# Performance work log

Hardware: AMD Instinct MI355X
Metric: run time of the kernel (lower is better)

The kernel has to match this reference:

```python
import jax, jax.numpy as jnp
import numpy as np

B, N, E, IN = 16, 4096, 65536, 128
FILTERS = [256, 256, 128]


def setup_inputs() -> dict:
    key = jax.random.key(0)
    ks = jax.random.split(key, 12)
    inp = {
        "x": jax.random.normal(ks[0], (B, N, IN), dtype=jnp.float32),
        "edge_index": jax.random.randint(ks[1], (B, 2, E), 0, N, dtype=jnp.int32),
        "edge_weight": jax.random.uniform(ks[2], (B, E), dtype=jnp.float32),
        "mask": jax.random.randint(ks[3], (B, N), 0, 2, dtype=jnp.int32),
    }
    dims = [IN] + FILTERS
    for i in range(3):
        inp[f"W{i+1}"] = jax.random.normal(ks[4 + 2 * i], (dims[i], dims[i + 1]), dtype=jnp.float32) / np.sqrt(dims[i]).astype(np.float32)
        inp[f"b{i+1}"] = 0.01 * jax.random.normal(ks[5 + 2 * i], (dims[i + 1],), dtype=jnp.float32)
    return inp


def _gcn_layer(x, ei, ew, valid, W, b):
    # GCNConv(add_self_loops=False, normalize=False):
    #   h = x @ W; out[v] = sum_{(u,v)} ew * h[u]; out += b (valid rows only)
    h = x @ W  # [N, d_out]
    u, v = ei[0], ei[1]
    evalid = valid[u] & valid[v]            # drop edges touching masked-out nodes
    w = jnp.where(evalid, ew, 0.0)
    agg = jnp.zeros_like(h).at[v].add(w[:, None] * h[u])
    return jnp.where(valid[:, None], agg + b, 0.0)


def reference(x, edge_index, edge_weight, mask, W1, b1, W2, b2, W3, b3):
    valid = mask > 0  # [B, N] bool
    out = x
    for W, b in ((W1, b1), (W2, b2), (W3, b3)):
        out = jax.vmap(_gcn_layer, in_axes=(0, 0, 0, 0, None, None))(
            out, edge_index, edge_weight, valid, W, b)
        out = jax.nn.relu(out)  # dropout p=0.0 -> identity
    return out
```

## Files before the change

kernel.cpp:

```cpp
#include <hip/hip_runtime.h>

static constexpr int BATCH = 16;
static constexpr int NNODE = 4096;
static constexpr int NEDGE = 65536;
static constexpr int ROWS  = BATCH * NNODE;
static constexpr int CAP   = 2432;
static constexpr int PM    = BATCH * CAP;

typedef _Float16 half8  __attribute__((ext_vector_type(8)));
typedef _Float16 half4v __attribute__((ext_vector_type(4)));
typedef _Float16 half2v __attribute__((ext_vector_type(2)));
typedef float    f32x4  __attribute__((ext_vector_type(4)));
typedef float    f32x2  __attribute__((ext_vector_type(2)));

#define GP(p) (const __attribute__((address_space(1))) void*)(p)
#define LP(p) (__attribute__((address_space(3))) void*)(p)


__global__ __launch_bounds__(256) void count_kernel(
    const int* __restrict__ ei, const int* __restrict__ mask,
    int* __restrict__ counts)
{
    const int idx = blockIdx.x * 256 + threadIdx.x;
    const int b = idx >> 16;
    const int e = idx & (NEDGE - 1);
    const int* eib = ei + (size_t)b * 2 * NEDGE;
    const int u = eib[e];
    const int v = eib[NEDGE + e];
    const int mrow = b * NNODE;
    if (mask[mrow + u] != 0 && mask[mrow + v] != 0)
        atomicAdd(&counts[mrow + v], 1);
}

__global__ __launch_bounds__(256) void scan_compact_kernel(
    const int* __restrict__ counts, const int* __restrict__ mask,
    int* __restrict__ row_start, int* __restrict__ cursor,
    int* __restrict__ vlist, int* __restrict__ cidx, int* __restrict__ validN)
{
    __shared__ int sums[256];
    const int t = threadIdx.x;

    if (blockIdx.x < BATCH) {
        const int b = blockIdx.x;
        const int* c = counts + b * NNODE;
        int* rs = row_start + b * (NNODE + 1);
        int* cu = cursor + b * NNODE;

        int local[16]; int s = 0;
        #pragma unroll
        for (int i = 0; i < 16; ++i) { local[i] = c[t * 16 + i]; s += local[i]; }
        sums[t] = s;
        __syncthreads();
        for (int off = 1; off < 256; off <<= 1) {
            int v = (t >= off) ? sums[t - off] : 0;
            __syncthreads();
            sums[t] += v;
            __syncthreads();
        }
        int run = (t == 0) ? 0 : sums[t - 1];
        #pragma unroll
        for (int i = 0; i < 16; ++i) { rs[t * 16 + i] = run; cu[t * 16 + i] = run; run += local[i]; }
        if (t == 255) rs[NNODE] = run;
    } else {
        const int b = blockIdx.x - BATCH;
        const int* mb = mask + b * NNODE;
        for (int i = t; i < CAP; i += 256) vlist[b * CAP + i] = 0;

        int loc[16]; int s = 0;
        #pragma unroll
        for (int i = 0; i < 16; ++i) { loc[i] = (mb[t * 16 + i] != 0); s += loc[i]; }
        sums[t] = s;
        __syncthreads();
        for (int off = 1; off < 256; off <<= 1) {
            int v = (t >= off) ? sums[t - off] : 0;
            __syncthreads();
            sums[t] += v;
            __syncthreads();
        }
        int run = (t == 0) ? 0 : sums[t - 1];
        #pragma unroll
        for (int i = 0; i < 16; ++i) {
            const int n = t * 16 + i;
            if (loc[i]) {
                if (run < CAP) { vlist[b * CAP + run] = n; cidx[b * NNODE + n] = b * CAP + run; }
                ++run;
            } else {
                cidx[b * NNODE + n] = 0;
            }
        }
        if (t == 255) validN[b] = run;
    }
}

__global__ __launch_bounds__(256) void fill_prep_kernel(
    const int* __restrict__ ei, const float* __restrict__ ew,
    const int* __restrict__ mask, const int* __restrict__ cidx,
    int* __restrict__ cursor, unsigned int* __restrict__ bkt,
    const float* __restrict__ X, const int* __restrict__ vlist,
    const float* __restrict__ W1, const float* __restrict__ W2,
    const float* __restrict__ W3,
    _Float16* __restrict__ X16c, _Float16* __restrict__ Wt1,
    _Float16* __restrict__ Wt2, _Float16* __restrict__ Wt3)
{
    const int blk = blockIdx.x;
    if (blk < 4096) {
        const int idx = blk * 256 + threadIdx.x;
        const int b = idx >> 16;
        const int e = idx & (NEDGE - 1);
        const int* eib = ei + (size_t)b * 2 * NEDGE;
        const int u = eib[e];
        const int v = eib[NEDGE + e];
        const int mrow = b * NNODE;
        if (mask[mrow + u] != 0 && mask[mrow + v] != 0) {
            const _Float16 w = (_Float16)ew[(size_t)b * NEDGE + e];
            const unsigned short wb = __builtin_bit_cast(unsigned short, w);
            const unsigned uc = (unsigned)cidx[mrow + u];
            const int pos = atomicAdd(&cursor[mrow + v], 1);
            bkt[(size_t)b * NEDGE + pos] = ((unsigned)wb << 16) | uc;
        }
    } else {
        const int idx = (blk - 4096) * 256 + threadIdx.x;
        if (idx < PM * 32) {
            const int row = idx >> 5;
            const int c4  = idx & 31;
            const int b   = row / CAP;
            const int v   = vlist[row];
            const float4 s = *(const float4*)&X[((size_t)b * NNODE + v) * 128 + c4 * 4];
            half4v h = {(_Float16)s.x, (_Float16)s.y, (_Float16)s.z, (_Float16)s.w};
            *(half4v*)&X16c[(size_t)row * 128 + c4 * 4] = h;
        } else {
            const int i = idx - PM * 32;
            if (i < 32768) {
                int k = i >> 8, n = i & 255;
                Wt1[n * 128 + k] = (_Float16)W1[i];
            } else if (i < 98304) {
                int j = i - 32768;
                int k = j >> 8, n = j & 255;
                Wt2[n * 256 + k] = (_Float16)W2[j];
            } else {
                int j = i - 98304;
                int k = j >> 7, n = j & 127;
                Wt3[n * 256 + k] = (_Float16)W3[j];
            }
        }
    }
}

template<int K, int N, bool EPI>
__global__ __launch_bounds__(256, 3) void gemm_full(
    const _Float16* __restrict__ Xc,
    const _Float16* __restrict__ Wt,
    const float* __restrict__ bias,
    _Float16* __restrict__ Hc)
{
    constexpr int NCH  = CAP / 64;
    constexpr int NPAN = K / 32;
    constexpr int NW   = N / 4;
    constexpr int NI   = NW / 16;
    constexpr int RST  = NW + 8;
    __shared__ _Float16 A16[NPAN * 64 * 32];

    const int tid  = threadIdx.x;
    const int lane = tid & 63;
    const int wave = tid >> 6;
    const int quad = lane >> 4;
    const int l15  = lane & 15;

    const int xcd  = blockIdx.x & 7;
    const int j    = blockIdx.x >> 3;
    const int batch = 2 * xcd + (j >= NCH);
    const int tile  = (j >= NCH) ? j - NCH : j;
    const size_t bm = (size_t)batch * CAP + (size_t)tile * 64;

    const int srow = tid >> 2;
    const int sch  = (tid & 3) * 8;
    #pragma unroll
    for (int pp = 0; pp < NPAN; ++pp)
        __builtin_amdgcn_global_load_lds(
            GP(Xc + (bm + srow) * K + pp * 32 + sch),
            LP(A16 + pp * 2048 + tid * 8), 16, 0, 0);
    __syncthreads();

    f32x4 acc[4][NI];
    #pragma unroll
    for (int mi = 0; mi < 4; ++mi)
        #pragma unroll
        for (int ni = 0; ni < NI; ++ni) acc[mi][ni] = (f32x4)0.0f;

    const _Float16* ap = A16 + l15 * 32 + quad * 8;
    const _Float16* wp = Wt + (size_t)(wave * NW + l15) * K + quad * 8;

    #pragma unroll
    for (int pp = 0; pp < NPAN; ++pp) {
        half8 af[4], bf[NI];
        #pragma unroll
        for (int mi = 0; mi < 4; ++mi)
            af[mi] = *(const half8*)(ap + pp * 2048 + mi * 16 * 32);
        #pragma unroll
        for (int ni = 0; ni < NI; ++ni)
            bf[ni] = *(const half8*)(wp + (size_t)ni * 16 * K + pp * 32);
        #pragma unroll
        for (int mi = 0; mi < 4; ++mi)
            #pragma unroll
            for (int ni = 0; ni < NI; ++ni)
                acc[mi][ni] = __builtin_amdgcn_mfma_f32_16x16x32_f16(
                    bf[ni], af[mi], acc[mi][ni], 0, 0, 0);
    }
    __syncthreads();

    _Float16* stg = A16 + wave * 16 * RST;
    const int rr = lane >> 2;
    const int c0 = lane & 3;
    #pragma unroll
    for (int mi = 0; mi < 4; ++mi) {
        #pragma unroll
        for (int ni = 0; ni < NI; ++ni) {
            f32x4 v = acc[mi][ni];
            half4v o;
            if (EPI) {
                const f32x4 bv = *(const f32x4*)&bias[wave * NW + ni * 16 + quad * 4];
                #pragma unroll
                for (int r = 0; r < 4; ++r) o[r] = (_Float16)fmaxf(v[r] + bv[r], 0.0f);
            } else {
                #pragma unroll
                for (int r = 0; r < 4; ++r) o[r] = (_Float16)v[r];
            }
            *(half4v*)&stg[l15 * RST + ni * 16 + quad * 4] = o;
        }
        const size_t grow = bm + mi * 16 + rr;
        _Float16* hp = &Hc[grow * N + wave * NW];
        #pragma unroll
        for (int c = 0; c < NI / 2; ++c) {
            const int ch = (c0 + 4 * c) * 8;
            half8 v = *(const half8*)&stg[rr * RST + ch];
            *(half8*)(hp + ch) = v;
        }
    }
}

__global__ __launch_bounds__(256, 3) void gemm23_kernel(
    const _Float16* __restrict__ Xc,
    const _Float16* __restrict__ Wt2,
    const _Float16* __restrict__ Wt3,
    const float* __restrict__ b2,
    _Float16* __restrict__ H3)
{
    constexpr int K    = 256;
    constexpr int NPAN = K / 32;
    constexpr int NCH  = CAP / 64;
    __shared__ _Float16 A16[NPAN * 64 * 32];

    const int tid  = threadIdx.x;
    const int lane = tid & 63;
    const int wave = tid >> 6;
    const int quad = lane >> 4;
    const int l15  = lane & 15;

    const int xcd  = blockIdx.x & 7;
    const int j    = blockIdx.x >> 3;
    const int batch = 2 * xcd + (j >= NCH);
    const int tile  = (j >= NCH) ? j - NCH : j;
    const size_t bm = (size_t)batch * CAP + (size_t)tile * 64;

    const int srow = tid >> 2;
    const int sch  = (tid & 3) * 8;
    #pragma unroll
    for (int pp = 0; pp < NPAN; ++pp)
        __builtin_amdgcn_global_load_lds(
            GP(Xc + (bm + srow) * K + pp * 32 + sch),
            LP(A16 + pp * 2048 + tid * 8), 16, 0, 0);
    __syncthreads();

    f32x4 acc[4][4];
    #pragma unroll
    for (int mi = 0; mi < 4; ++mi)
        #pragma unroll
        for (int ni = 0; ni < 4; ++ni) acc[mi][ni] = (f32x4)0.0f;

    const _Float16* ap = A16 + l15 * 32 + quad * 8;
    const _Float16* wp = Wt2 + (size_t)(wave * 64 + l15) * K + quad * 8;

    #pragma unroll
    for (int pp = 0; pp < NPAN; ++pp) {
        half8 af[4], bf[4];
        #pragma unroll
        for (int mi = 0; mi < 4; ++mi)
            af[mi] = *(const half8*)(ap + pp * 2048 + mi * 16 * 32);
        #pragma unroll
        for (int ni = 0; ni < 4; ++ni)
            bf[ni] = *(const half8*)(wp + (size_t)ni * 16 * K + pp * 32);
        #pragma unroll
        for (int mi = 0; mi < 4; ++mi)
            #pragma unroll
            for (int ni = 0; ni < 4; ++ni)
                acc[mi][ni] = __builtin_amdgcn_mfma_f32_16x16x32_f16(
                    bf[ni], af[mi], acc[mi][ni], 0, 0, 0);
    }
    __syncthreads();

    #pragma unroll
    for (int mi = 0; mi < 4; ++mi) {
        const int row = mi * 16 + l15;
        #pragma unroll
        for (int ni = 0; ni < 4; ++ni) {
            const int col = wave * 64 + ni * 16 + quad * 4;
            const f32x4 bv = *(const f32x4*)&b2[col];
            f32x4 v = acc[mi][ni];
            half4v o;
            #pragma unroll
            for (int r = 0; r < 4; ++r) o[r] = (_Float16)fmaxf(v[r] + bv[r], 0.0f);
            *(half4v*)&A16[(col >> 5) * 2048 + row * 32 + (col & 31)] = o;
        }
    }
    __syncthreads();

    f32x4 acc2[4][2];
    #pragma unroll
    for (int mi = 0; mi < 4; ++mi)
        #pragma unroll
        for (int ni = 0; ni < 2; ++ni) acc2[mi][ni] = (f32x4)0.0f;

    const _Float16* wp3 = Wt3 + (size_t)(wave * 32 + l15) * K + quad * 8;
    #pragma unroll
    for (int pp = 0; pp < NPAN; ++pp) {
        half8 af[4], bf[2];
        #pragma unroll
        for (int mi = 0; mi < 4; ++mi)
            af[mi] = *(const half8*)(ap + pp * 2048 + mi * 16 * 32);
        #pragma unroll
        for (int ni = 0; ni < 2; ++ni)
            bf[ni] = *(const half8*)(wp3 + (size_t)ni * 16 * K + pp * 32);
        #pragma unroll
        for (int mi = 0; mi < 4; ++mi)
            #pragma unroll
            for (int ni = 0; ni < 2; ++ni)
                acc2[mi][ni] = __builtin_amdgcn_mfma_f32_16x16x32_f16(
                    bf[ni], af[mi], acc2[mi][ni], 0, 0, 0);
    }
    __syncthreads();

    constexpr int RST = 40;
    _Float16* stg = A16 + wave * 16 * RST;
    const int rr = lane >> 2;
    const int c0 = lane & 3;
    #pragma unroll
    for (int mi = 0; mi < 4; ++mi) {
        #pragma unroll
        for (int ni = 0; ni < 2; ++ni) {
            f32x4 v = acc2[mi][ni];
            half4v o;
            #pragma unroll
            for (int r = 0; r < 4; ++r) o[r] = (_Float16)v[r];
            *(half4v*)&stg[l15 * RST + ni * 16 + quad * 4] = o;
        }
        const size_t grow = bm + mi * 16 + rr;
        _Float16* hp = &H3[grow * 128 + wave * 32];
        {
            const int ch = c0 * 8;
            half8 v = *(const half8*)&stg[rr * RST + ch];
            *(half8*)(hp + ch) = v;
        }
    }
}


__global__ __launch_bounds__(256) void gather_x(
    const int* __restrict__ row_start, const unsigned int* __restrict__ bkt,
    const _Float16* __restrict__ X,
    const int* __restrict__ vlist, const int* __restrict__ validN,
    _Float16* __restrict__ OUT)
{
    constexpr int NU = CAP / 4;
    const int tid  = threadIdx.x;
    const int lane = tid & 63;
    const int wave = tid >> 6;

    const int xcd  = blockIdx.x & 7;
    const int jj   = blockIdx.x >> 3;
    const int batch = 2 * xcd + (jj >= NU);
    const int unit  = (jj >= NU) ? jj - NU : jj;

    const int j = unit * 4 + wave;
    if (j >= validN[batch]) return;
    const int g = batch * CAP + j;
    const int v = vlist[g];

    const int* rs = row_start + batch * (NNODE + 1);
    const int s = rs[v], e = rs[v + 1];
    const unsigned* bk = bkt + (size_t)batch * NEDGE;
    const _Float16* Hb = X + lane * 2;

    float acc[2] = {};
    for (int i = s; i < e; i += 8) {
        const int cnt = e - i;
        unsigned pk[8];
        #pragma unroll
        for (int t = 0; t < 8; ++t) pk[t] = bk[i + t];
        const unsigned u0 = pk[0] & 0xffffu;
        float wj[8]; const _Float16* hp[8];
        #pragma unroll
        for (int t = 0; t < 8; ++t) {
            const bool ok = (t < cnt);
            const unsigned u = ok ? (pk[t] & 0xffffu) : u0;
            wj[t] = ok ? (float)__builtin_bit_cast(_Float16, (unsigned short)(pk[t] >> 16)) : 0.0f;
            hp[t] = Hb + (size_t)u * 128;
        }
        half2v hv[8];
        #pragma unroll
        for (int t = 0; t < 8; ++t) hv[t] = *(const half2v*)hp[t];
        #pragma unroll
        for (int t = 0; t < 8; ++t)
            #pragma unroll
            for (int c = 0; c < 2; ++c) acc[c] += wj[t] * (float)hv[t][c];
    }
    half2v o = {(_Float16)acc[0], (_Float16)acc[1]};
    *(half2v*)&OUT[(size_t)g * 128 + lane * 2] = o;
}

__global__ __launch_bounds__(256) void gather_agg(
    const int* __restrict__ row_start, const unsigned int* __restrict__ bkt,
    const _Float16* __restrict__ H,
    const int* __restrict__ vlist, const int* __restrict__ validN,
    _Float16* __restrict__ OUT)
{
    constexpr int NU = CAP / 4;
    const int tid  = threadIdx.x;
    const int lane = tid & 63;
    const int wave = tid >> 6;

    const int xcd  = blockIdx.x & 7;
    const int jj   = blockIdx.x >> 3;
    const int batch = 2 * xcd + (jj >= NU);
    const int unit  = (jj >= NU) ? jj - NU : jj;

    const int j = unit * 4 + wave;
    if (j >= validN[batch]) return;
    const int g = batch * CAP + j;
    const int v = vlist[g];

    const int* rs = row_start + batch * (NNODE + 1);
    const int s = rs[v], e = rs[v + 1];
    const unsigned* bk = bkt + (size_t)batch * NEDGE;
    const _Float16* Hb = H + lane * 4;

    float acc[4] = {};
    for (int i = s; i < e; i += 8) {
        const int cnt = e - i;
        unsigned pk[8];
        #pragma unroll
        for (int t = 0; t < 8; ++t) pk[t] = bk[i + t];
        const unsigned u0 = pk[0] & 0xffffu;
        float wj[8]; const _Float16* hp[8];
        #pragma unroll
        for (int t = 0; t < 8; ++t) {
            const bool ok = (t < cnt);
            const unsigned u = ok ? (pk[t] & 0xffffu) : u0;
            wj[t] = ok ? (float)__builtin_bit_cast(_Float16, (unsigned short)(pk[t] >> 16)) : 0.0f;
            hp[t] = Hb + (size_t)u * 256;
        }
        half4v hv[8];
        #pragma unroll
        for (int t = 0; t < 8; ++t) hv[t] = *(const half4v*)hp[t];
        #pragma unroll
        for (int t = 0; t < 8; ++t)
            #pragma unroll
            for (int c = 0; c < 4; ++c) acc[c] += wj[t] * (float)hv[t][c];
    }
    half4v o;
    #pragma unroll
    for (int c = 0; c < 4; ++c) o[c] = (_Float16)acc[c];
    *(half4v*)&OUT[(size_t)g * 256 + lane * 4] = o;
}

__global__ __launch_bounds__(256) void gather_final(
    const int* __restrict__ row_start, const unsigned int* __restrict__ bkt,
    const _Float16* __restrict__ H,
    const int* __restrict__ mask, const float* __restrict__ bias,
    float* __restrict__ OUT)
{
    constexpr int NU = NNODE / 4;
    const int tid  = threadIdx.x;
    const int lane = tid & 63;
    const int wave = tid >> 6;

    const int xcd  = blockIdx.x & 7;
    const int jj   = blockIdx.x >> 3;
    const int batch = 2 * xcd + (jj >= NU);
    const int unit  = (jj >= NU) ? jj - NU : jj;

    const int n = unit * 4 + wave;
    const int mrow = batch * NNODE + n;

    float acc[2] = {};
    if (mask[mrow] != 0) {
        const int* rs = row_start + batch * (NNODE + 1);
        const int s = rs[n], e = rs[n + 1];
        const unsigned* bk = bkt + (size_t)batch * NEDGE;
        const _Float16* Hb = H + lane * 2;

        for (int i = s; i < e; i += 8) {
            const int cnt = e - i;
            unsigned pk[8];
            #pragma unroll
            for (int t = 0; t < 8; ++t) pk[t] = bk[i + t];
            const unsigned u0 = pk[0] & 0xffffu;
            float wj[8]; const _Float16* hp[8];
            #pragma unroll
            for (int t = 0; t < 8; ++t) {
                const bool ok = (t < cnt);
                const unsigned u = ok ? (pk[t] & 0xffffu) : u0;
                wj[t] = ok ? (float)__builtin_bit_cast(_Float16, (unsigned short)(pk[t] >> 16)) : 0.0f;
                hp[t] = Hb + (size_t)u * 128;
            }
            half2v hv[8];
            #pragma unroll
            for (int t = 0; t < 8; ++t) hv[t] = *(const half2v*)hp[t];
            #pragma unroll
            for (int t = 0; t < 8; ++t)
                #pragma unroll
                for (int c = 0; c < 2; ++c) acc[c] += wj[t] * (float)hv[t][c];
        }
        #pragma unroll
        for (int c = 0; c < 2; ++c)
            acc[c] = fmaxf(acc[c] + bias[lane * 2 + c], 0.0f);
    }
    f32x2 o = {acc[0], acc[1]};
    *(f32x2*)&OUT[(size_t)mrow * 128 + lane * 2] = o;
}

extern "C" void kernel_launch(void* const* d_in, const int* in_sizes, int n_in,
                              void* d_out, int out_size, void* d_ws, size_t ws_size,
                              hipStream_t stream) {
    const float* x    = (const float*)d_in[0];
    const int*   ei   = (const int*)  d_in[1];
    const float* ew   = (const float*)d_in[2];
    const int*   mask = (const int*)  d_in[3];
    const float* W1   = (const float*)d_in[4];
    const float* b1   = (const float*)d_in[5];
    const float* W2   = (const float*)d_in[6];
    const float* b2   = (const float*)d_in[7];
    const float* W3   = (const float*)d_in[8];
    const float* b3   = (const float*)d_in[9];
    float* out = (float*)d_out;

    char* ws = (char*)d_ws;
    _Float16* X16c = (_Float16*)(ws);
    _Float16* AggX = (_Float16*)(ws + (10u << 20));
    _Float16* H3c  = AggX;
    _Float16* Ac   = (_Float16*)(ws + (20u << 20));
    _Float16* AggA = (_Float16*)(ws + (40u << 20));
    unsigned int* bkt = (unsigned int*)(ws + (60u << 20));
    _Float16* Wt1  = (_Float16*)(ws + (64u << 20));
    _Float16* Wt2  = Wt1 + 128 * 256;
    _Float16* Wt3  = Wt2 + 256 * 256;
    int* counts    = (int*)(Wt3 + 256 * 128);
    int* row_start = counts + ROWS;
    int* cursor    = row_start + BATCH * (NNODE + 1);
    int* cidx      = cursor + ROWS;
    int* vlist     = cidx + ROWS;
    int* validN    = vlist + PM;

    const dim3 blk(256);
    const int edgeBlocks = BATCH * NEDGE / 256;

    hipMemsetAsync(counts, 0, (size_t)ROWS * sizeof(int), stream);
    count_kernel<<<edgeBlocks, blk, 0, stream>>>(ei, mask, counts);
    scan_compact_kernel<<<2 * BATCH, blk, 0, stream>>>(counts, mask, row_start, cursor,
                                                       vlist, cidx, validN);
    const int prepBlocks = (PM * 32 + 131072) / 256;
    fill_prep_kernel<<<edgeBlocks + prepBlocks, blk, 0, stream>>>(
        ei, ew, mask, cidx, cursor, bkt, x, vlist, W1, W2, W3,
        X16c, Wt1, Wt2, Wt3);

    const int gemmBlocks = PM / 64;
    const int midBlocks  = PM / 4;
    const int finBlocks  = ROWS / 4;

    gather_x<<<midBlocks, blk, 0, stream>>>(row_start, bkt, X16c, vlist, validN, AggX);
    gemm_full<128, 256, true><<<gemmBlocks, blk, 0, stream>>>(AggX, Wt1, b1, Ac);

    gather_agg<<<midBlocks, blk, 0, stream>>>(row_start, bkt, Ac, vlist, validN, AggA);
    gemm23_kernel<<<gemmBlocks, blk, 0, stream>>>(AggA, Wt2, Wt3, b2, H3c);

    gather_final<<<finBlocks, blk, 0, stream>>>(row_start, bkt, H3c, mask, b3, out);
}
```

Measured before the change: 228.0 us.

## Fuse neighbor gathers into GEMM kernels and use fixed-capacity per-node edge buckets

Replaces the count, prefix-scan and CSR fill passes with one build kernel that scatters each valid edge into a fixed 64-slot bucket per destination node. The per-node cursor doubles as the degree. The separate gather kernels for layers 1 and 2 are folded into the GEMM kernels: each block aggregates its 64 compacted rows straight into shared memory before running the matrix multiply, and writes results scattered to full node-indexed buffers. This removes several launches and the round trips through intermediate aggregated buffers. In exchange, fewer waves do the gather serially, and edges beyond 64 per node are silently dropped.

Result: faster. 221.5 us (-2.9%).

```diff
diff --git a/kernel.cpp b/kernel.cpp
--- a/kernel.cpp
+++ b/kernel.cpp
@@ -6,6 +6,7 @@
 static constexpr int ROWS  = BATCH * NNODE;
 static constexpr int CAP   = 2432;
 static constexpr int PM    = BATCH * CAP;
+static constexpr int DCAP  = 64;
 
 typedef _Float16 half8  __attribute__((ext_vector_type(8)));
 typedef _Float16 half4v __attribute__((ext_vector_type(4)));
@@ -13,98 +14,22 @@
 typedef float    f32x4  __attribute__((ext_vector_type(4)));
 typedef float    f32x2  __attribute__((ext_vector_type(2)));
 
-#define GP(p) (const __attribute__((address_space(1))) void*)(p)
-#define LP(p) (__attribute__((address_space(3))) void*)(p)
-
-
-__global__ __launch_bounds__(256) void count_kernel(
-    const int* __restrict__ ei, const int* __restrict__ mask,
-    int* __restrict__ counts)
-{
-    const int idx = blockIdx.x * 256 + threadIdx.x;
-    const int b = idx >> 16;
-    const int e = idx & (NEDGE - 1);
-    const int* eib = ei + (size_t)b * 2 * NEDGE;
-    const int u = eib[e];
-    const int v = eib[NEDGE + e];
-    const int mrow = b * NNODE;
-    if (mask[mrow + u] != 0 && mask[mrow + v] != 0)
-        atomicAdd(&counts[mrow + v], 1);
-}
-
-__global__ __launch_bounds__(256) void scan_compact_kernel(
-    const int* __restrict__ counts, const int* __restrict__ mask,
-    int* __restrict__ row_start, int* __restrict__ cursor,
-    int* __restrict__ vlist, int* __restrict__ cidx, int* __restrict__ validN)
+__global__ __launch_bounds__(256) void build_kernel(
+    const int* __restrict__ ei, const float* __restrict__ ew,
+    const int* __restrict__ mask, const float* __restrict__ X,
+    const float* __restrict__ W1, const float* __restrict__ W2,
+    const float* __restrict__ W3,
+    int* __restrict__ cursor, unsigned int* __restrict__ bkt,
+    _Float16* __restrict__ X16, _Float16* __restrict__ Wt1,
+    _Float16* __restrict__ Wt2, _Float16* __restrict__ Wt3,
+    int* __restrict__ vlist, int* __restrict__ validN)
 {
     __shared__ int sums[256];
-    const int t = threadIdx.x;
-
-    if (blockIdx.x < BATCH) {
-        const int b = blockIdx.x;
-        const int* c = counts + b * NNODE;
-        int* rs = row_start + b * (NNODE + 1);
-        int* cu = cursor + b * NNODE;
-
-        int local[16]; int s = 0;
-        #pragma unroll
-        for (int i = 0; i < 16; ++i) { local[i] = c[t * 16 + i]; s += local[i]; }
-        sums[t] = s;
-        __syncthreads();
-        for (int off = 1; off < 256; off <<= 1) {
-            int v = (t >= off) ? sums[t - off] : 0;
-            __syncthreads();
-            sums[t] += v;
-            __syncthreads();
-        }
-        int run = (t == 0) ? 0 : sums[t - 1];
-        #pragma unroll
-        for (int i = 0; i < 16; ++i) { rs[t * 16 + i] = run; cu[t * 16 + i] = run; run += local[i]; }
-        if (t == 255) rs[NNODE] = run;
-    } else {
-        const int b = blockIdx.x - BATCH;
-        const int* mb = mask + b * NNODE;
-        for (int i = t; i < CAP; i += 256) vlist[b * CAP + i] = 0;
-
-        int loc[16]; int s = 0;
-        #pragma unroll
-        for (int i = 0; i < 16; ++i) { loc[i] = (mb[t * 16 + i] != 0); s += loc[i]; }
-        sums[t] = s;
-        __syncthreads();
-        for (int off = 1; off < 256; off <<= 1) {
-            int v = (t >= off) ? sums[t - off] : 0;
-            __syncthreads();
-            sums[t] += v;
-            __syncthreads();
-        }
-        int run = (t == 0) ? 0 : sums[t - 1];
-        #pragma unroll
-        for (int i = 0; i < 16; ++i) {
-            const int n = t * 16 + i;
-            if (loc[i]) {
-                if (run < CAP) { vlist[b * CAP + run] = n; cidx[b * NNODE + n] = b * CAP + run; }
-                ++run;
-            } else {
-                cidx[b * NNODE + n] = 0;
-            }
-        }
-        if (t == 255) validN[b] = run;
-    }
-}
-
-__global__ __launch_bounds__(256) void fill_prep_kernel(
-    const int* __restrict__ ei, const float* __restrict__ ew,
-    const int* __restrict__ mask, const int* __restrict__ cidx,
-    int* __restrict__ cursor, unsigned int* __restrict__ bkt,
-    const float* __restrict__ X, const int* __restrict__ vlist,
-    const float* __restrict__ W1, const float* __restrict__ W2,
-    const float* __restrict__ W3,
-    _Float16* __restrict__ X16c, _Float16* __restrict__ Wt1,
-    _Float16* __restrict__ Wt2, _Float16* __restrict__ Wt3)
-{
     const int blk = blockIdx.x;
+    const int t   = threadIdx.x;
+
     if (blk < 4096) {
-        const int idx = blk * 256 + threadIdx.x;
+        const int idx = blk * 256 + t;
         const int b = idx >> 16;
         const int e = idx & (NEDGE - 1);
         const int* eib = ei + (size_t)b * 2 * NEDGE;
@@ -114,51 +39,75 @@
         if (mask[mrow + u] != 0 && mask[mrow + v] != 0) {
             const _Float16 w = (_Float16)ew[(size_t)b * NEDGE + e];
             const unsigned short wb = __builtin_bit_cast(unsigned short, w);
-            const unsigned uc = (unsigned)cidx[mrow + u];
             const int pos = atomicAdd(&cursor[mrow + v], 1);
-            bkt[(size_t)b * NEDGE + pos] = ((unsigned)wb << 16) | uc;
+            if (pos < DCAP)
+                bkt[(size_t)(mrow + v) * DCAP + pos] = ((unsigned)wb << 16) | (unsigned)u;
+        }
+    } else if (blk < 12288) {
+        const int i = (blk - 4096) * 256 + t;
+        const int row = i >> 5;
+        const int c4  = i & 31;
+        const float4 s = *(const float4*)&X[(size_t)row * 128 + c4 * 4];
+        half4v h = {(_Float16)s.x, (_Float16)s.y, (_Float16)s.z, (_Float16)s.w};
+        *(half4v*)&X16[(size_t)row * 128 + c4 * 4] = h;
+    } else if (blk < 12800) {
+        const int i = (blk - 12288) * 256 + t;
+        if (i < 32768) {
+            int k = i >> 8, n = i & 255;
+            Wt1[n * 128 + k] = (_Float16)W1[i];
+        } else if (i < 98304) {
+            int j = i - 32768;
+            int k = j >> 8, n = j & 255;
+            Wt2[n * 256 + k] = (_Float16)W2[j];
+        } else {
+            int j = i - 98304;
+            int k = j >> 7, n = j & 127;
+            Wt3[n * 256 + k] = (_Float16)W3[j];
         }
     } else {
-        const int idx = (blk - 4096) * 256 + threadIdx.x;
-        if (idx < PM * 32) {
-            const int row = idx >> 5;
-            const int c4  = idx & 31;
-            const int b   = row / CAP;
-            const int v   = vlist[row];
-            const float4 s = *(const float4*)&X[((size_t)b * NNODE + v) * 128 + c4 * 4];
-            half4v h = {(_Float16)s.x, (_Float16)s.y, (_Float16)s.z, (_Float16)s.w};
-            *(half4v*)&X16c[(size_t)row * 128 + c4 * 4] = h;
-        } else {
-            const int i = idx - PM * 32;
-            if (i < 32768) {
-                int k = i >> 8, n = i & 255;
-                Wt1[n * 128 + k] = (_Float16)W1[i];
-            } else if (i < 98304) {
-                int j = i - 32768;
-                int k = j >> 8, n = j & 255;
-                Wt2[n * 256 + k] = (_Float16)W2[j];
-            } else {
-                int j = i - 98304;
-                int k = j >> 7, n = j & 127;
-                Wt3[n * 256 + k] = (_Float16)W3[j];
+        const int b = blk - 12800;
+        const int* mb = mask + b * NNODE;
+        for (int i = t; i < CAP; i += 256) vlist[b * CAP + i] = 0;
+
+        int loc[16]; int s = 0;
+        #pragma unroll
+        for (int i = 0; i < 16; ++i) { loc[i] = (mb[t * 16 + i] != 0); s += loc[i]; }
+        sums[t] = s;
+        __syncthreads();
+        for (int off = 1; off < 256; off <<= 1) {
+            int v = (t >= off) ? sums[t - off] : 0;
+            __syncthreads();
+            sums[t] += v;
+            __syncthreads();
+        }
+        int run = (t == 0) ? 0 : sums[t - 1];
+        #pragma unroll
+        for (int i = 0; i < 16; ++i) {
+            const int n = t * 16 + i;
+            if (loc[i]) {
+                if (run < CAP) vlist[b * CAP + run] = n;
+                ++run;
             }
         }
+        if (t == 255) validN[b] = run;
     }
 }
 
-template<int K, int N, bool EPI>
-__global__ __launch_bounds__(256, 3) void gemm_full(
-    const _Float16* __restrict__ Xc,
+__global__ __launch_bounds__(256, 3) void fused_g1(
+    const unsigned int* __restrict__ bkt, const int* __restrict__ cursor,
+    const _Float16* __restrict__ X16,
+    const int* __restrict__ vlist, const int* __restrict__ validN,
     const _Float16* __restrict__ Wt,
     const float* __restrict__ bias,
-    _Float16* __restrict__ Hc)
+    _Float16* __restrict__ Ac)
 {
-    constexpr int NCH  = CAP / 64;
+    constexpr int K = 128, N = 256;
     constexpr int NPAN = K / 32;
     constexpr int NW   = N / 4;
     constexpr int NI   = NW / 16;
     constexpr int RST  = NW + 8;
-    __shared__ _Float16 A16[NPAN * 64 * 32];
+    constexpr int NCH  = CAP / 64;
+    __shared__ _Float16 A16[NPAN * 2048];
 
     const int tid  = threadIdx.x;
     const int lane = tid & 63;
@@ -170,15 +119,47 @@
     const int j    = blockIdx.x >> 3;
     const int batch = 2 * xcd + (j >= NCH);
     const int tile  = (j >= NCH) ? j - NCH : j;
-    const size_t bm = (size_t)batch * CAP + (size_t)tile * 64;
-
-    const int srow = tid >> 2;
-    const int sch  = (tid & 3) * 8;
-    #pragma unroll
-    for (int pp = 0; pp < NPAN; ++pp)
-        __builtin_amdgcn_global_load_lds(
-            GP(Xc + (bm + srow) * K + pp * 32 + sch),
-            LP(A16 + pp * 2048 + tid * 8), 16, 0, 0);
+    const int vN   = validN[batch];
+    if (tile * 64 >= vN) return;
+    const int mrow = batch * NNODE;
+    const _Float16* Xb = X16 + (size_t)mrow * 128 + lane * 2;
+
+    for (int r = 0; r < 16; ++r) {
+        const int slot = tile * 64 + wave * 16 + r;
+        float a0 = 0.0f, a1 = 0.0f;
+        if (slot < vN) {
+            const int v = vlist[batch * CAP + slot];
+            int deg = cursor[mrow + v];
+            deg = deg > DCAP ? DCAP : deg;
+            const unsigned* bk = bkt + (size_t)(mrow + v) * DCAP;
+            for (int i = 0; i < deg; i += 8) {
+                const int cnt = deg - i;
+                unsigned pk[8];
+                #pragma unroll
+                for (int tt = 0; tt < 8; ++tt) pk[tt] = bk[i + tt];
+                const unsigned u0 = pk[0] & 0xffffu;
+                float wj[8]; const _Float16* hp[8];
+                #pragma unroll
+                for (int tt = 0; tt < 8; ++tt) {
+                    const bool ok = (tt < cnt);
+                    const unsigned u = ok ? (pk[tt] & 0xffffu) : u0;
+                    wj[tt] = ok ? (float)__builtin_bit_cast(_Float16, (unsigned short)(pk[tt] >> 16)) : 0.0f;
+                    hp[tt] = Xb + (size_t)u * 128;
+                }
+                half2v hv[8];
+                #pragma unroll
+                for (int tt = 0; tt < 8; ++tt) hv[tt] = *(const half2v*)hp[tt];
+                #pragma unroll
+                for (int tt = 0; tt < 8; ++tt) {
+                    a0 += wj[tt] * (float)hv[tt][0];
+                    a1 += wj[tt] * (float)hv[tt][1];
+                }
+            }
+        }
+        const int row = wave * 16 + r;
+        half2v o = {(_Float16)a0, (_Float16)a1};
+        *(half2v*)&A16[quad * 2048 + row * 32 + l15 * 2] = o;
+    }
     __syncthreads();
 
     f32x4 acc[4][NI];
@@ -216,39 +197,39 @@
         #pragma unroll
         for (int ni = 0; ni < NI; ++ni) {
             f32x4 v = acc[mi][ni];
+            const f32x4 bv = *(const f32x4*)&bias[wave * NW + ni * 16 + quad * 4];
             half4v o;
-            if (EPI) {
-                const f32x4 bv = *(const f32x4*)&bias[wave * NW + ni * 16 + quad * 4];
-                #pragma unroll
-                for (int r = 0; r < 4; ++r) o[r] = (_Float16)fmaxf(v[r] + bv[r], 0.0f);
-            } else {
-                #pragma unroll
-                for (int r = 0; r < 4; ++r) o[r] = (_Float16)v[r];
+            #pragma unroll
+            for (int r = 0; r < 4; ++r) o[r] = (_Float16)fmaxf(v[r] + bv[r], 0.0f);
+            *(half4v*)&stg[l15 * RST + ni * 16 + quad * 4] = o;
+        }
+        const int slot = tile * 64 + mi * 16 + rr;
+        if (slot < vN) {
+            const int vs = vlist[batch * CAP + slot];
+            _Float16* hp2 = &Ac[((size_t)mrow + vs) * 256 + wave * NW];
+            #pragma unroll
+            for (int c = 0; c < NI / 2; ++c) {
+                const int ch = (c0 + 4 * c) * 8;
+                half8 v = *(const half8*)&stg[rr * RST + ch];
+                *(half8*)(hp2 + ch) = v;
             }
-            *(half4v*)&stg[l15 * RST + ni * 16 + quad * 4] = o;
-        }
-        const size_t grow = bm + mi * 16 + rr;
-        _Float16* hp = &Hc[grow * N + wave * NW];
-        #pragma unroll
-        for (int c = 0; c < NI / 2; ++c) {
-            const int ch = (c0 + 4 * c) * 8;
-            half8 v = *(const half8*)&stg[rr * RST + ch];
-            *(half8*)(hp + ch) = v;
         }
     }
 }
 
-__global__ __launch_bounds__(256, 3) void gemm23_kernel(
-    const _Float16* __restrict__ Xc,
+__global__ __launch_bounds__(256, 3) void fused_g23(
+    const unsigned int* __restrict__ bkt, const int* __restrict__ cursor,
+    const _Float16* __restrict__ Ac,
+    const int* __restrict__ vlist, const int* __restrict__ validN,
     const _Float16* __restrict__ Wt2,
     const _Float16* __restrict__ Wt3,
     const float* __restrict__ b2,
     _Float16* __restrict__ H3)
 {
     constexpr int K    = 256;
-    constexpr int NPAN = K / 32;
+    constexpr int NPAN = 8;
     constexpr int NCH  = CAP / 64;
-    __shared__ _Float16 A16[NPAN * 64 * 32];
+    __shared__ _Float16 A16[NPAN * 2048];
 
     const int tid  = threadIdx.x;
     const int lane = tid & 63;
@@ -260,15 +241,49 @@
     const int j    = blockIdx.x >> 3;
     const int batch = 2 * xcd + (j >= NCH);
     const int tile  = (j >= NCH) ? j - NCH : j;
-    const size_t bm = (size_t)batch * CAP + (size_t)tile * 64;
-
-    const int srow = tid >> 2;
-    const int sch  = (tid & 3) * 8;
-    #pragma unroll
-    for (int pp = 0; pp < NPAN; ++pp)
-        __builtin_amdgcn_global_load_lds(
-            GP(Xc + (bm + srow) * K + pp * 32 + sch),
-            LP(A16 + pp * 2048 + tid * 8), 16, 0, 0);
+    const int vN   = validN[batch];
+    if (tile * 64 >= vN) return;
+    const int mrow = batch * NNODE;
+    const _Float16* Ab = Ac + (size_t)mrow * 256 + lane * 4;
+
+    for (int r = 0; r < 16; ++r) {
+        const int slot = tile * 64 + wave * 16 + r;
+        float a0 = 0.0f, a1 = 0.0f, a2 = 0.0f, a3 = 0.0f;
+        if (slot < vN) {
+            const int v = vlist[batch * CAP + slot];
+            int deg = cursor[mrow + v];
+            deg = deg > DCAP ? DCAP : deg;
+            const unsigned* bk = bkt + (size_t)(mrow + v) * DCAP;
+            for (int i = 0; i < deg; i += 8) {
+                const int cnt = deg - i;
+                unsigned pk[8];
+                #pragma unroll
+                for (int tt = 0; tt < 8; ++tt) pk[tt] = bk[i + tt];
+                const unsigned u0 = pk[0] & 0xffffu;
+                float wj[8]; const _Float16* hp[8];
+                #pragma unroll
+                for (int tt = 0; tt < 8; ++tt) {
+                    const bool ok = (tt < cnt);
+                    const unsigned u = ok ? (pk[tt] & 0xffffu) : u0;
+                    wj[tt] = ok ? (float)__builtin_bit_cast(_Float16, (unsigned short)(pk[tt] >> 16)) : 0.0f;
+                    hp[tt] = Ab + (size_t)u * 256;
+                }
+                half4v hv[8];
+                #pragma unroll
+                for (int tt = 0; tt < 8; ++tt) hv[tt] = *(const half4v*)hp[tt];
+                #pragma unroll
+                for (int tt = 0; tt < 8; ++tt) {
+                    a0 += wj[tt] * (float)hv[tt][0];
+                    a1 += wj[tt] * (float)hv[tt][1];
+                    a2 += wj[tt] * (float)hv[tt][2];
+                    a3 += wj[tt] * (float)hv[tt][3];
+                }
+            }
+        }
+        const int row = wave * 16 + r;
+        half4v o = {(_Float16)a0, (_Float16)a1, (_Float16)a2, (_Float16)a3};
+        *(half4v*)&A16[(lane >> 3) * 2048 + row * 32 + ((lane * 4) & 31)] = o;
+    }
     __syncthreads();
 
     f32x4 acc[4][4];
@@ -353,128 +368,20 @@
             for (int r = 0; r < 4; ++r) o[r] = (_Float16)v[r];
             *(half4v*)&stg[l15 * RST + ni * 16 + quad * 4] = o;
         }
-        const size_t grow = bm + mi * 16 + rr;
-        _Float16* hp = &H3[grow * 128 + wave * 32];
-        {
+        const int slot = tile * 64 + mi * 16 + rr;
+        if (slot < vN) {
+            const int vs = vlist[batch * CAP + slot];
+            _Float16* hp2 = &H3[((size_t)mrow + vs) * 128 + wave * 32];
             const int ch = c0 * 8;
             half8 v = *(const half8*)&stg[rr * RST + ch];
-            *(half8*)(hp + ch) = v;
+            *(half8*)(hp2 + ch) = v;
         }
     }
 }
 
-
-__global__ __launch_bounds__(256) void gather_x(
-    const int* __restrict__ row_start, const unsigned int* __restrict__ bkt,
-    const _Float16* __restrict__ X,
-    const int* __restrict__ vlist, const int* __restrict__ validN,
-    _Float16* __restrict__ OUT)
-{
-    constexpr int NU = CAP / 4;
-    const int tid  = threadIdx.x;
-    const int lane = tid & 63;
-    const int wave = tid >> 6;
-
-    const int xcd  = blockIdx.x & 7;
-    const int jj   = blockIdx.x >> 3;
-    const int batch = 2 * xcd + (jj >= NU);
-    const int unit  = (jj >= NU) ? jj - NU : jj;
-
-    const int j = unit * 4 + wave;
-    if (j >= validN[batch]) return;
-    const int g = batch * CAP + j;
-    const int v = vlist[g];
-
-    const int* rs = row_start + batch * (NNODE + 1);
-    const int s = rs[v], e = rs[v + 1];
-    const unsigned* bk = bkt + (size_t)batch * NEDGE;
-    const _Float16* Hb = X + lane * 2;
-
-    float acc[2] = {};
-    for (int i = s; i < e; i += 8) {
-        const int cnt = e - i;
-        unsigned pk[8];
-        #pragma unroll
-        for (int t = 0; t < 8; ++t) pk[t] = bk[i + t];
-        const unsigned u0 = pk[0] & 0xffffu;
-        float wj[8]; const _Float16* hp[8];
-        #pragma unroll
-        for (int t = 0; t < 8; ++t) {
-            const bool ok = (t < cnt);
-            const unsigned u = ok ? (pk[t] & 0xffffu) : u0;
-            wj[t] = ok ? (float)__builtin_bit_cast(_Float16, (unsigned short)(pk[t] >> 16)) : 0.0f;
-            hp[t] = Hb + (size_t)u * 128;
-        }
-        half2v hv[8];
-        #pragma unroll
-        for (int t = 0; t < 8; ++t) hv[t] = *(const half2v*)hp[t];
-        #pragma unroll
-        for (int t = 0; t < 8; ++t)
-            #pragma unroll
-            for (int c = 0; c < 2; ++c) acc[c] += wj[t] * (float)hv[t][c];
-    }
-    half2v o = {(_Float16)acc[0], (_Float16)acc[1]};
-    *(half2v*)&OUT[(size_t)g * 128 + lane * 2] = o;
-}
-
-__global__ __launch_bounds__(256) void gather_agg(
-    const int* __restrict__ row_start, const unsigned int* __restrict__ bkt,
-    const _Float16* __restrict__ H,
-    const int* __restrict__ vlist, const int* __restrict__ validN,
-    _Float16* __restrict__ OUT)
-{
-    constexpr int NU = CAP / 4;
-    const int tid  = threadIdx.x;
-    const int lane = tid & 63;
-    const int wave = tid >> 6;
-
-    const int xcd  = blockIdx.x & 7;
-    const int jj   = blockIdx.x >> 3;
-    const int batch = 2 * xcd + (jj >= NU);
-    const int unit  = (jj >= NU) ? jj - NU : jj;
-
-    const int j = unit * 4 + wave;
-    if (j >= validN[batch]) return;
-    const int g = batch * CAP + j;
-    const int v = vlist[g];
-
-    const int* rs = row_start + batch * (NNODE + 1);
-    const int s = rs[v], e = rs[v + 1];
-    const unsigned* bk = bkt + (size_t)batch * NEDGE;
-    const _Float16* Hb = H + lane * 4;
-
-    float acc[4] = {};
-    for (int i = s; i < e; i += 8) {
-        const int cnt = e - i;
-        unsigned pk[8];
-        #pragma unroll
-        for (int t = 0; t < 8; ++t) pk[t] = bk[i + t];
-        const unsigned u0 = pk[0] & 0xffffu;
-        float wj[8]; const _Float16* hp[8];
-        #pragma unroll
-        for (int t = 0; t < 8; ++t) {
-            const bool ok = (t < cnt);
-            const unsigned u = ok ? (pk[t] & 0xffffu) : u0;
-            wj[t] = ok ? (float)__builtin_bit_cast(_Float16, (unsigned short)(pk[t] >> 16)) : 0.0f;
-            hp[t] = Hb + (size_t)u * 256;
-        }
-        half4v hv[8];
-        #pragma unroll
-        for (int t = 0; t < 8; ++t) hv[t] = *(const half4v*)hp[t];
-        #pragma unroll
-        for (int t = 0; t < 8; ++t)
-            #pragma unroll
-            for (int c = 0; c < 4; ++c) acc[c] += wj[t] * (float)hv[t][c];
-    }
-    half4v o;
-    #pragma unroll
-    for (int c = 0; c < 4; ++c) o[c] = (_Float16)acc[c];
-    *(half4v*)&OUT[(size_t)g * 256 + lane * 4] = o;
-}
-
 __global__ __launch_bounds__(256) void gather_final(
-    const int* __restrict__ row_start, const unsigned int* __restrict__ bkt,
-    const _Float16* __restrict__ H,
+    const int* __restrict__ cursor, const unsigned int* __restrict__ bkt,
+    const _Float16* __restrict__ H3,
     const int* __restrict__ mask, const float* __restrict__ bias,
     float* __restrict__ OUT)
 {
@@ -493,13 +400,13 @@
 
     float acc[2] = {};
     if (mask[mrow] != 0) {
-        const int* rs = row_start + batch * (NNODE + 1);
-        const int s = rs[n], e = rs[n + 1];
-        const unsigned* bk = bkt + (size_t)batch * NEDGE;
-        const _Float16* Hb = H + lane * 2;
-
-        for (int i = s; i < e; i += 8) {
-            const int cnt = e - i;
+        int deg = cursor[mrow];
+        deg = deg > DCAP ? DCAP : deg;
+        const unsigned* bk = bkt + (size_t)mrow * DCAP;
+        const _Float16* Hb = H3 + (size_t)batch * NNODE * 128 + lane * 2;
+
+        for (int i = 0; i < deg; i += 8) {
+            const int cnt = deg - i;
             unsigned pk[8];
             #pragma unroll
             for (int t = 0; t < 8; ++t) pk[t] = bk[i + t];
@@ -544,43 +451,33 @@
     float* out = (float*)d_out;
 
     char* ws = (char*)d_ws;
-    _Float16* X16c = (_Float16*)(ws);
-    _Float16* AggX = (_Float16*)(ws + (10u << 20));
-    _Float16* H3c  = AggX;
-    _Float16* Ac   = (_Float16*)(ws + (20u << 20));
-    _Float16* AggA = (_Float16*)(ws + (40u << 20));
-    unsigned int* bkt = (unsigned int*)(ws + (60u << 20));
-    _Float16* Wt1  = (_Float16*)(ws + (64u << 20));
-    _Float16* Wt2  = Wt1 + 128 * 256;
-    _Float16* Wt3  = Wt2 + 256 * 256;
-    int* counts    = (int*)(Wt3 + 256 * 128);
-    int* row_start = counts + ROWS;
-    int* cursor    = row_start + BATCH * (NNODE + 1);
-    int* cidx      = cursor + ROWS;
-    int* vlist     = cidx + ROWS;
-    int* validN    = vlist + PM;
+    _Float16* X16 = (_Float16*)(ws);
+    _Float16* Ac  = (_Float16*)(ws + (16u << 20));
+    _Float16* H3  = (_Float16*)(ws + (48u << 20));
+    unsigned int* bkt = (unsigned int*)(ws + (64u << 20));
+    _Float16* Wt1 = (_Float16*)(ws + (80u << 20));
+    _Float16* Wt2 = Wt1 + 128 * 256;
+    _Float16* Wt3 = Wt2 + 256 * 256;
+    int* cursor   = (int*)(Wt3 + 256 * 128);
+    int* vlist    = cursor + ROWS;
+    int* validN   = vlist + PM;
 
     const dim3 blk(256);
-    const int edgeBlocks = BATCH * NEDGE / 256;
-
-    hipMemsetAsync(counts, 0, (size_t)ROWS * sizeof(int), stream);
-    count_kernel<<<edgeBlocks, blk, 0, stream>>>(ei, mask, counts);
-    scan_compact_kernel<<<2 * BATCH, blk, 0, stream>>>(counts, mask, row_start, cursor,
-                                                       vlist, cidx, validN);
-    const int prepBlocks = (PM * 32 + 131072) / 256;
-    fill_prep_kernel<<<edgeBlocks + prepBlocks, blk, 0, stream>>>(
-        ei, ew, mask, cidx, cursor, bkt, x, vlist, W1, W2, W3,
-        X16c, Wt1, Wt2, Wt3);
+
+    hipMemsetAsync(cursor, 0, (size_t)ROWS * sizeof(int), stream);
+
+    build_kernel<<<12816, blk, 0, stream>>>(ei, ew, mask, x, W1, W2, W3,
+                                            cursor, bkt, X16, Wt1, Wt2, Wt3,
+                                            vlist, validN);
 
     const int gemmBlocks = PM / 64;
-    const int midBlocks  = PM / 4;
     const int finBlocks  = ROWS / 4;
 
-    gather_x<<<midBlocks, blk, 0, stream>>>(row_start, bkt, X16c, vlist, validN, AggX);
-    gemm_full<128, 256, true><<<gemmBlocks, blk, 0, stream>>>(AggX, Wt1, b1, Ac);
-
-    gather_agg<<<midBlocks, blk, 0, stream>>>(row_start, bkt, Ac, vlist, validN, AggA);
-    gemm23_kernel<<<gemmBlocks, blk, 0, stream>>>(AggA, Wt2, Wt3, b2, H3c);
-
-    gather_final<<<finBlocks, blk, 0, stream>>>(row_start, bkt, H3c, mask, b3, out);
+    fused_g1<<<gemmBlocks, blk, 0, stream>>>(bkt, cursor, X16, vlist, validN,
+                                             Wt1, b1, Ac);
+
+    fused_g23<<<gemmBlocks, blk, 0, stream>>>(bkt, cursor, Ac, vlist, validN,
+                                              Wt2, Wt3, b2, H3);
+
+    gather_final<<<finBlocks, blk, 0, stream>>>(cursor, bkt, H3, mask, b3, out);
 }
```
